# Optimization experiments

Hardware: AMD Instinct MI355X
Metric: run time of the kernel (lower is better)

Reference implementation:

```python
import jax, jax.numpy as jnp
import numpy as np

D = 256; NH = 8; NL = 4; NP = 4; DFF = 2048; HD = D // NH
SHAPES = [(64, 64), (32, 32), (16, 16), (8, 8)]
B = 2; LEN = sum(h * w for h, w in SHAPES)


def setup_inputs() -> dict:
    key = jax.random.key(0)
    ks = jax.random.split(key, 12)
    def w(k, shape, s=0.02):
        return jax.random.normal(k, shape, jnp.float32) * s
    starts = np.cumsum([0] + [h * w for h, w in SHAPES[:-1]])
    return {
        "src": jax.random.normal(ks[0], (B, LEN, D), jnp.float32),
        "pos": jax.random.normal(ks[1], (B, LEN, D), jnp.float32) * 0.1,
        "spatial_shapes": jnp.array(SHAPES, dtype=jnp.int32),
        "level_start_index": jnp.array(starts, dtype=jnp.int32),
        "w_value": w(ks[2], (D, D)), "b_value": jnp.zeros((D,), jnp.float32),
        "w_off": w(ks[3], (D, NH * NL * NP * 2)), "b_off": w(ks[4], (NH * NL * NP * 2,), 0.1),
        "w_attn": w(ks[5], (D, NH * NL * NP)), "b_attn": jnp.zeros((NH * NL * NP,), jnp.float32),
        "w_out": w(ks[6], (D, D)), "b_out": jnp.zeros((D,), jnp.float32),
        "w1": w(ks[7], (D, DFF)), "b1": jnp.zeros((DFF,), jnp.float32),
        "w2": w(ks[8], (DFF, D)), "b2": jnp.zeros((D,), jnp.float32),
        "g1": jnp.ones((D,), jnp.float32), "be1": jnp.zeros((D,), jnp.float32),
        "g2": jnp.ones((D,), jnp.float32), "be2": jnp.zeros((D,), jnp.float32),
    }


def _layer_norm(x, g, b):
    mu = jnp.mean(x, -1, keepdims=True)
    v = jnp.var(x, -1, keepdims=True)
    return (x - mu) * jax.lax.rsqrt(v + 1e-5) * g + b


def _reference_points(shapes):
    # torch.linspace(0.5, H-0.5, H)/H == (arange(H)+0.5)/H
    refs = []
    for H, W in shapes:
        ry = (jnp.arange(H, dtype=jnp.float32) + 0.5) / H
        rx = (jnp.arange(W, dtype=jnp.float32) + 0.5) / W
        yy, xx = jnp.meshgrid(ry, rx, indexing='ij')
        refs.append(jnp.stack([xx.ravel(), yy.ravel()], -1))
    return jnp.concatenate(refs, 0)  # (Len, 2) as (x, y)


def _ms_deform_sample(value, loc, shapes):
    # value: (B, Len, NH, HD); loc: (B, Lq, NH, NL, NP, 2) normalized [0,1]
    # Replicates torch grid_sample(bilinear, padding='zeros', align_corners=False).
    Bn, Lq = loc.shape[0], loc.shape[1]
    P = loc.shape[4]
    start = 0
    outs = []
    for lvl, (H, W) in enumerate(shapes):
        v = value[:, start:start + H * W].transpose(0, 2, 1, 3)  # (B, NH, HW, HD)
        start += H * W
        l = loc[:, :, :, lvl]                      # (B, Lq, NH, P, 2)
        x = l[..., 0] * W - 0.5
        y = l[..., 1] * H - 0.5
        x0 = jnp.floor(x); y0 = jnp.floor(y)
        dx = x - x0; dy = y - y0
        x0i = x0.astype(jnp.int32); y0i = y0.astype(jnp.int32)
        acc = None
        for xi, yi, wgt in ((x0i, y0i, (1 - dx) * (1 - dy)),
                            (x0i + 1, y0i, dx * (1 - dy)),
                            (x0i, y0i + 1, (1 - dx) * dy),
                            (x0i + 1, y0i + 1, dx * dy)):
            valid = ((xi >= 0) & (xi < W) & (yi >= 0) & (yi < H)).astype(value.dtype)
            idx = jnp.clip(yi, 0, H - 1) * W + jnp.clip(xi, 0, W - 1)  # (B, Lq, NH, P)
            idx = idx.transpose(0, 2, 1, 3).reshape(Bn, NH, Lq * P)
            g = jnp.take_along_axis(v, idx[..., None], axis=2).reshape(Bn, NH, Lq, P, HD)
            w = (wgt * valid).transpose(0, 2, 1, 3)[..., None]  # (B, NH, Lq, P, 1)
            acc = g * w if acc is None else acc + g * w
        outs.append(acc)  # (B, NH, Lq, P, HD)
    return jnp.stack(outs, 3)  # (B, NH, Lq, NL, NP, HD)


def _forward(src, pos, w_value, b_value, w_off, b_off, w_attn, b_attn,
             w_out, b_out, w1, b1, w2, b2, g1, be1, g2, be2, shapes):
    Bn, Lq, _ = src.shape
    q = src + pos  # with_pos_embed
    value = (src @ w_value + b_value).reshape(Bn, Lq, NH, HD)
    off = (q @ w_off + b_off).reshape(Bn, Lq, NH, NL, NP, 2)
    attn = jax.nn.softmax((q @ w_attn + b_attn).reshape(Bn, Lq, NH, NL * NP), -1)
    attn = attn.reshape(Bn, Lq, NH, NL, NP)
    ref = _reference_points(shapes)  # (Len, 2)
    normalizer = jnp.array([[w_, h_] for h_, w_ in shapes], jnp.float32)  # (NL, 2) = (W, H)
    loc = ref[None, :, None, None, None, :] + off / normalizer[None, None, None, :, None, :]
    sampled = _ms_deform_sample(value, loc, shapes)  # (B, NH, Lq, NL, NP, HD)
    out = jnp.einsum('bqhlp,bhqlpd->bqhd', attn, sampled).reshape(Bn, Lq, D)
    out = out @ w_out + b_out
    x = _layer_norm(src + out, g1, be1)           # residual + norm1
    ff = jax.nn.relu(x @ w1 + b1) @ w2 + b2       # FFN (dropout=0)
    return _layer_norm(x + ff, g2, be2)           # residual + norm2


def reference(src, pos, spatial_shapes, level_start_index, w_value, b_value,
              w_off, b_off, w_attn, b_attn, w_out, b_out, w1, b1, w2, b2,
              g1, be1, g2, be2):
    shapes = [tuple(int(v) for v in s) for s in np.asarray(spatial_shapes)]
    return _forward(src, pos, w_value, b_value, w_off, b_off, w_attn, b_attn,
                    w_out, b_out, w1, b1, w2, b2, g1, be1, g2, be2, shapes)
```

## Files before the change

### kernel.cpp

```cpp
#include <hip/hip_runtime.h>
#include <math.h>

#define D 256
#define NH 8
#define NL 4
#define NP 4
#define DFF 2048
#define HD 32
#define BB 2
#define LEN 5440
#define MROWS (BB * LEN)

typedef __attribute__((ext_vector_type(8))) short short8;
typedef __attribute__((ext_vector_type(4))) float f32x4;
typedef unsigned int uint32;

__device__ __forceinline__ unsigned short f2bf(float f) {
    uint32 u = __float_as_uint(f);
    u += 0x7FFF + ((u >> 16) & 1);
    return (unsigned short)(u >> 16);
}
__device__ __forceinline__ float bf2f(unsigned short h) {
    return __uint_as_float(((uint32)h) << 16);
}
__device__ __forceinline__ uint32 pack2(float a, float b) {
    return (uint32)f2bf(a) | ((uint32)f2bf(b) << 16);
}

__device__ __forceinline__ void swz85(int b, int ncols, int& row, int& col) {
    const int gsz = ncols << 3;
    const int full = 10 * gsz;
    if (b < full) {
        const int g = b / gsz, idx = b - g * gsz;
        row = (g << 3) + (idx & 7);
        col = idx >> 3;
    } else {
        const int idx = b - full;
        row = 80 + idx % 5;
        col = idx / 5;
    }
}

__global__ void prep(const float* __restrict__ w_value, const float* __restrict__ w_off,
                     const float* __restrict__ w_attn, const float* __restrict__ w_out,
                     const float* __restrict__ w1, const float* __restrict__ w2,
                     const float* __restrict__ b_value, const float* __restrict__ b_off,
                     const float* __restrict__ b_attn,
                     unsigned short* __restrict__ wqvT, unsigned short* __restrict__ woT,
                     unsigned short* __restrict__ w1T, unsigned short* __restrict__ w2T,
                     float* __restrict__ bqv) {
    const int blk = blockIdx.x;
    if (blk >= 1248) {
        for (int i = threadIdx.x; i < 640; i += 256)
            bqv[i] = (i < 256) ? b_value[i] : (i < 512 ? b_off[i - 256] : b_attn[i - 512]);
        return;
    }
    const float* W; unsigned short* WT; int K, N, tid;
    if (blk < 64)       { W = w_value; WT = wqvT;             K = 256;  N = 256;  tid = blk; }
    else if (blk < 128) { W = w_off;   WT = wqvT + 256 * 256; K = 256;  N = 256;  tid = blk - 64; }
    else if (blk < 160) { W = w_attn;  WT = wqvT + 512 * 256; K = 256;  N = 128;  tid = blk - 128; }
    else if (blk < 224) { W = w_out;   WT = woT;              K = 256;  N = 256;  tid = blk - 160; }
    else if (blk < 736) { W = w1;      WT = w1T;              K = 256;  N = 2048; tid = blk - 224; }
    else                { W = w2;      WT = w2T;              K = 2048; N = 256;  tid = blk - 736; }
    const int ntx = N >> 5;
    const int nb = (tid % ntx) * 32, kb = (tid / ntx) * 32;

    __shared__ float tile[32][33];
    const int tx = threadIdx.x & 31, ty = threadIdx.x >> 5;
#pragma unroll
    for (int i = 0; i < 32; i += 8)
        tile[ty + i][tx] = W[(size_t)(kb + ty + i) * N + nb + tx];
    __syncthreads();
#pragma unroll
    for (int i = 0; i < 32; i += 8)
        WT[(size_t)(nb + ty + i) * K + kb + tx] = f2bf(tile[tx][ty + i]);
}

__global__ __launch_bounds__(256) void ffn1_gemm(
        const unsigned short* __restrict__ A,
        const unsigned short* __restrict__ BT, const float* __restrict__ bias,
        unsigned short* __restrict__ Cv, int N, int K, int lda, int ldb) {
    __shared__ unsigned short Ash[128][40];
    __shared__ unsigned short Bsh[128][40];

    int rowt, colt;
    swz85(blockIdx.x, N >> 7, rowt, colt);
    const int row0 = rowt * 128, col0 = colt * 128;

    const int t = threadIdx.x;
    const int wave = t >> 6, lane = t & 63;
    const int wr = wave >> 1, wc = wave & 1;
    const int lrow = lane & 15, quad = lane >> 4;
    const int srow = t >> 1;
    const int cb = (t & 1) * 16;

    const unsigned short* ap = A + (size_t)(row0 + srow) * lda + cb;
    const unsigned short* bp = BT + (size_t)(col0 + srow) * ldb + cb;

    f32x4 acc[4][4];
#pragma unroll
    for (int i = 0; i < 4; i++)
#pragma unroll
        for (int j = 0; j < 4; j++) acc[i][j] = (f32x4){0.f, 0.f, 0.f, 0.f};

    uint4 ra0 = *(const uint4*)(ap + 0), ra1 = *(const uint4*)(ap + 8);
    uint4 rb0 = *(const uint4*)(bp + 0), rb1 = *(const uint4*)(bp + 8);

    for (int kb = 0; kb < K; kb += 32) {
        __syncthreads();
        *(uint4*)&Ash[srow][cb + 0] = ra0;
        *(uint4*)&Ash[srow][cb + 8] = ra1;
        *(uint4*)&Bsh[srow][cb + 0] = rb0;
        *(uint4*)&Bsh[srow][cb + 8] = rb1;
        __syncthreads();
        if (kb + 32 < K) {
            ra0 = *(const uint4*)(ap + kb + 32 + 0);
            ra1 = *(const uint4*)(ap + kb + 32 + 8);
            rb0 = *(const uint4*)(bp + kb + 32 + 0);
            rb1 = *(const uint4*)(bp + kb + 32 + 8);
        }

        short8 af[4], bfr[4];
#pragma unroll
        for (int mt = 0; mt < 4; mt++)
            af[mt] = *(const short8*)&Ash[wr * 64 + mt * 16 + lrow][quad * 8];
#pragma unroll
        for (int nt = 0; nt < 4; nt++)
            bfr[nt] = *(const short8*)&Bsh[wc * 64 + nt * 16 + lrow][quad * 8];
#pragma unroll
        for (int mt = 0; mt < 4; mt++)
#pragma unroll
            for (int nt = 0; nt < 4; nt++)
                acc[mt][nt] = __builtin_amdgcn_mfma_f32_16x16x32_bf16(
                    af[mt], bfr[nt], acc[mt][nt], 0, 0, 0);
    }

#pragma unroll
    for (int nt = 0; nt < 4; nt++) {
        const int col = col0 + wc * 64 + nt * 16 + lrow;
        const float bv = bias[col];
#pragma unroll
        for (int mt = 0; mt < 4; mt++) {
            f32x4 a = acc[mt][nt];
#pragma unroll
            for (int r = 0; r < 4; r++) {
                const int row = row0 + wr * 64 + mt * 16 + quad * 4 + r;
                Cv[(size_t)row * N + col] = f2bf(fmaxf(a[r] + bv, 0.f));
            }
        }
    }
}

template <bool WRITE16>
__global__ __launch_bounds__(256) void gemm_ln(
        const unsigned short* __restrict__ A, const unsigned short* __restrict__ BT,
        const float* __restrict__ bias, const float* __restrict__ rsd,
        const float* __restrict__ g, const float* __restrict__ be,
        float* __restrict__ out, unsigned short* __restrict__ out16, int K) {
    __shared__ __align__(16) unsigned short Ash[32][40];
    __shared__ __align__(16) unsigned short Bsh[256][40];
    __shared__ float red1[4][32], red2[4][32];

    const int row0 = blockIdx.x * 32;
    const int t = threadIdx.x;
    const int wave = t >> 6, lane = t & 63;
    const int lrow = lane & 15, quad = lane >> 4;

    const int ar = t >> 3, ac = (t & 7) * 4;
    const unsigned short* ap = A + (size_t)(row0 + ar) * K + ac;
    const int br = t >> 1, cb = (t & 1) * 16;
    const unsigned short* bp0 = BT + (size_t)br * K + cb;
    const unsigned short* bp1 = BT + (size_t)(128 + br) * K + cb;

    f32x4 acc[2][4];
#pragma unroll
    for (int i = 0; i < 2; i++)
#pragma unroll
        for (int j = 0; j < 4; j++) acc[i][j] = (f32x4){0.f, 0.f, 0.f, 0.f};

    uint2 ra = *(const uint2*)ap;
    uint4 rb00 = *(const uint4*)(bp0 + 0), rb01 = *(const uint4*)(bp0 + 8);
    uint4 rb10 = *(const uint4*)(bp1 + 0), rb11 = *(const uint4*)(bp1 + 8);

    for (int kb = 0; kb < K; kb += 32) {
        __syncthreads();
        *(uint2*)&Ash[ar][ac] = ra;
        *(uint4*)&Bsh[br][cb + 0] = rb00;
        *(uint4*)&Bsh[br][cb + 8] = rb01;
        *(uint4*)&Bsh[128 + br][cb + 0] = rb10;
        *(uint4*)&Bsh[128 + br][cb + 8] = rb11;
        __syncthreads();
        if (kb + 32 < K) {
            ra   = *(const uint2*)(ap + kb + 32);
            rb00 = *(const uint4*)(bp0 + kb + 32 + 0);
            rb01 = *(const uint4*)(bp0 + kb + 32 + 8);
            rb10 = *(const uint4*)(bp1 + kb + 32 + 0);
            rb11 = *(const uint4*)(bp1 + kb + 32 + 8);
        }

        short8 af[2], bfr[4];
#pragma unroll
        for (int mt = 0; mt < 2; mt++)
            af[mt] = *(const short8*)&Ash[mt * 16 + lrow][quad * 8];
#pragma unroll
        for (int nt = 0; nt < 4; nt++)
            bfr[nt] = *(const short8*)&Bsh[wave * 64 + nt * 16 + lrow][quad * 8];
#pragma unroll
        for (int mt = 0; mt < 2; mt++)
#pragma unroll
            for (int nt = 0; nt < 4; nt++)
                acc[mt][nt] = __builtin_amdgcn_mfma_f32_16x16x32_bf16(
                    af[mt], bfr[nt], acc[mt][nt], 0, 0, 0);
    }

    float gv[4], bev[4], bv[4];
#pragma unroll
    for (int nt = 0; nt < 4; nt++) {
        const int col = wave * 64 + nt * 16 + lrow;
        bv[nt] = bias[col];
        gv[nt] = g[col];
        bev[nt] = be[col];
    }

    float v[2][4][4];
#pragma unroll
    for (int mt = 0; mt < 2; mt++)
#pragma unroll
        for (int r = 0; r < 4; r++) {
            const int row = row0 + mt * 16 + quad * 4 + r;
#pragma unroll
            for (int nt = 0; nt < 4; nt++) {
                const int col = wave * 64 + nt * 16 + lrow;
                v[mt][nt][r] = acc[mt][nt][r] + bv[nt] + rsd[(size_t)row * 256 + col];
            }
        }

#pragma unroll
    for (int mt = 0; mt < 2; mt++)
#pragma unroll
        for (int r = 0; r < 4; r++) {
            float s1 = v[mt][0][r] + v[mt][1][r] + v[mt][2][r] + v[mt][3][r];
            float s2 = v[mt][0][r] * v[mt][0][r] + v[mt][1][r] * v[mt][1][r] +
                       v[mt][2][r] * v[mt][2][r] + v[mt][3][r] * v[mt][3][r];
#pragma unroll
            for (int o = 1; o < 16; o <<= 1) {
                s1 += __shfl_xor(s1, o, 16);
                s2 += __shfl_xor(s2, o, 16);
            }
            if (lrow == 0) {
                const int rr = mt * 16 + quad * 4 + r;
                red1[wave][rr] = s1;
                red2[wave][rr] = s2;
            }
        }
    __syncthreads();

#pragma unroll
    for (int mt = 0; mt < 2; mt++)
#pragma unroll
        for (int r = 0; r < 4; r++) {
            const int rr = mt * 16 + quad * 4 + r;
            const float su = red1[0][rr] + red1[1][rr] + red1[2][rr] + red1[3][rr];
            const float sq = red2[0][rr] + red2[1][rr] + red2[2][rr] + red2[3][rr];
            const float mean = su * (1.0f / 256.0f);
            const float var = fmaxf(sq * (1.0f / 256.0f) - mean * mean, 0.f);
            const float rstd = rsqrtf(var + 1e-5f);
            const size_t rowoff = (size_t)(row0 + rr) * 256;
#pragma unroll
            for (int nt = 0; nt < 4; nt++) {
                const int col = wave * 64 + nt * 16 + lrow;
                const float o = (v[mt][nt][r] - mean) * rstd * gv[nt] + bev[nt];
                out[rowoff + col] = o;
                if (WRITE16) out16[rowoff + col] = f2bf(o);
            }
        }
}

__global__ __launch_bounds__(256) void qv_gemm(
        const float* __restrict__ src, const float* __restrict__ pos,
        const unsigned short* __restrict__ BT, const float* __restrict__ bias,
        unsigned short* __restrict__ val, float* __restrict__ qout) {
    __shared__ unsigned short Ash[128][40];
    __shared__ unsigned short Bsh[128][40];

    int rowt, colt;
    swz85(blockIdx.x, 5, rowt, colt);
    const int row0 = rowt * 128, col0 = colt * 128;
    const bool addp = (col0 >= 256);

    const int t = threadIdx.x;
    const int wave = t >> 6, lane = t & 63;
    const int wr = wave >> 1, wc = wave & 1;
    const int lrow = lane & 15, quad = lane >> 4;
    const int srow = t >> 1;
    const int cb = (t & 1) * 16;

    const float* ap = src + (size_t)(row0 + srow) * 256 + cb;
    const float* pp = pos + (size_t)(row0 + srow) * 256 + cb;
    const unsigned short* bp = BT + (size_t)(col0 + srow) * 256 + cb;

    f32x4 acc[4][4];
#pragma unroll
    for (int i = 0; i < 4; i++)
#pragma unroll
        for (int j = 0; j < 4; j++) acc[i][j] = (f32x4){0.f, 0.f, 0.f, 0.f};

    float4 fa[4]; float4 fp[4]; uint4 rb0, rb1;
#pragma unroll
    for (int j = 0; j < 4; j++) fa[j] = *(const float4*)(ap + 4 * j);
    if (addp) {
#pragma unroll
        for (int j = 0; j < 4; j++) fp[j] = *(const float4*)(pp + 4 * j);
    }
    rb0 = *(const uint4*)(bp + 0);
    rb1 = *(const uint4*)(bp + 8);

    for (int kb = 0; kb < 256; kb += 32) {
        __syncthreads();
        {
            float4 f0 = fa[0], f1 = fa[1], f2 = fa[2], f3 = fa[3];
            if (addp) {
                f0.x += fp[0].x; f0.y += fp[0].y; f0.z += fp[0].z; f0.w += fp[0].w;
                f1.x += fp[1].x; f1.y += fp[1].y; f1.z += fp[1].z; f1.w += fp[1].w;
                f2.x += fp[2].x; f2.y += fp[2].y; f2.z += fp[2].z; f2.w += fp[2].w;
                f3.x += fp[3].x; f3.y += fp[3].y; f3.z += fp[3].z; f3.w += fp[3].w;
            }
            uint4 u0 = make_uint4(pack2(f0.x, f0.y), pack2(f0.z, f0.w),
                                  pack2(f1.x, f1.y), pack2(f1.z, f1.w));
            uint4 u1 = make_uint4(pack2(f2.x, f2.y), pack2(f2.z, f2.w),
                                  pack2(f3.x, f3.y), pack2(f3.z, f3.w));
            *(uint4*)&Ash[srow][cb + 0] = u0;
            *(uint4*)&Ash[srow][cb + 8] = u1;
            *(uint4*)&Bsh[srow][cb + 0] = rb0;
            *(uint4*)&Bsh[srow][cb + 8] = rb1;
        }
        __syncthreads();
        if (kb + 32 < 256) {
#pragma unroll
            for (int j = 0; j < 4; j++) fa[j] = *(const float4*)(ap + kb + 32 + 4 * j);
            if (addp) {
#pragma unroll
                for (int j = 0; j < 4; j++) fp[j] = *(const float4*)(pp + kb + 32 + 4 * j);
            }
            rb0 = *(const uint4*)(bp + kb + 32 + 0);
            rb1 = *(const uint4*)(bp + kb + 32 + 8);
        }

        short8 af[4], bfr[4];
#pragma unroll
        for (int mt = 0; mt < 4; mt++)
            af[mt] = *(const short8*)&Ash[wr * 64 + mt * 16 + lrow][quad * 8];
#pragma unroll
        for (int nt = 0; nt < 4; nt++)
            bfr[nt] = *(const short8*)&Bsh[wc * 64 + nt * 16 + lrow][quad * 8];
#pragma unroll
        for (int mt = 0; mt < 4; mt++)
#pragma unroll
            for (int nt = 0; nt < 4; nt++)
                acc[mt][nt] = __builtin_amdgcn_mfma_f32_16x16x32_bf16(
                    af[mt], bfr[nt], acc[mt][nt], 0, 0, 0);
    }

#pragma unroll
    for (int nt = 0; nt < 4; nt++) {
        const int col = col0 + wc * 64 + nt * 16 + lrow;
        const float bv = bias[col];
#pragma unroll
        for (int mt = 0; mt < 4; mt++) {
            f32x4 a = acc[mt][nt];
#pragma unroll
            for (int r = 0; r < 4; r++) {
                const int row = row0 + wr * 64 + mt * 16 + quad * 4 + r;
                float v = a[r] + bv;
                if (col < 256)
                    val[(size_t)row * 256 + col] = f2bf(v);
                else
                    qout[(size_t)row * 384 + (col - 256)] = v;
            }
        }
    }
}

__global__ void sampler(const unsigned short* __restrict__ val, const float* __restrict__ qout,
                        unsigned short* __restrict__ out) {
    __shared__ __align__(16) int   sIdx[2][128][4];
    __shared__ __align__(16) float sW[2][128][4];
    const int t = threadIdx.x;
    const int sub = t >> 7;
    const int tt = t & 127;
    const int bq = blockIdx.x * 2 + sub;
    const int b = bq / LEN, q = bq % LEN;

    {
        const int h = tt >> 4, p = tt & 15;
        const int l = p >> 2;

        float refx, refy;
        if (q < 4096) {
            int rq = q >> 6, cq = q & 63;
            refx = (cq + 0.5f) * (1.0f / 64.0f);
            refy = (rq + 0.5f) * (1.0f / 64.0f);
        } else if (q < 5120) {
            int qq = q - 4096;
            int rq = qq >> 5, cq = qq & 31;
            refx = (cq + 0.5f) * (1.0f / 32.0f);
            refy = (rq + 0.5f) * (1.0f / 32.0f);
        } else if (q < 5376) {
            int qq = q - 5120;
            int rq = qq >> 4, cq = qq & 15;
            refx = (cq + 0.5f) * (1.0f / 16.0f);
            refy = (rq + 0.5f) * (1.0f / 16.0f);
        } else {
            int qq = q - 5376;
            int rq = qq >> 3, cq = qq & 7;
            refx = (cq + 0.5f) * (1.0f / 8.0f);
            refy = (rq + 0.5f) * (1.0f / 8.0f);
        }

        float lv = qout[(size_t)bq * 384 + 256 + tt];
        float mx = lv;
#pragma unroll
        for (int o = 1; o < 16; o <<= 1) mx = fmaxf(mx, __shfl_xor(mx, o, 16));
        float e = expf(lv - mx);
        float s = e;
#pragma unroll
        for (int o = 1; o < 16; o <<= 1) s += __shfl_xor(s, o, 16);
        const float aw = e / s;

        const float ox = qout[(size_t)bq * 384 + h * 32 + p * 2 + 0];
        const float oy = qout[(size_t)bq * 384 + h * 32 + p * 2 + 1];

        const int LST[4] = {0, 4096, 5120, 5376};
        const int WW = 64 >> l;
        const float rw = 1.0f / (float)WW;

        float x = (refx + ox * rw) * (float)WW - 0.5f;
        float y = (refy + oy * rw) * (float)WW - 0.5f;
        float x0f = floorf(x), y0f = floorf(y);
        float dx = x - x0f, dy = y - y0f;
        int x0 = (int)x0f, y0 = (int)y0f;

        const int base = (b * LEN + LST[l]) * 256 + h * 32;
        int xs[2] = {x0, x0 + 1}, ys[2] = {y0, y0 + 1};
        float wx[2] = {1.f - dx, dx}, wy[2] = {1.f - dy, dy};
        int ic[4]; float wc4[4];
#pragma unroll
        for (int cy = 0; cy < 2; cy++)
#pragma unroll
            for (int cx = 0; cx < 2; cx++) {
                int xi = xs[cx], yi = ys[cy];
                bool vld = (xi >= 0) && (xi < WW) && (yi >= 0) && (yi < WW);
                int xc = min(max(xi, 0), WW - 1);
                int yc = min(max(yi, 0), WW - 1);
                ic[cy * 2 + cx] = base + (yc * WW + xc) * 256;
                wc4[cy * 2 + cx] = vld ? wx[cx] * wy[cy] * aw : 0.f;
            }
        *(int4*)&sIdx[sub][tt][0] = make_int4(ic[0], ic[1], ic[2], ic[3]);
        *(float4*)&sW[sub][tt][0] = make_float4(wc4[0], wc4[1], wc4[2], wc4[3]);
    }
    __syncthreads();

    const int h = tt >> 4, dp = tt & 15;
    const unsigned short* vald = val + 2 * dp;
    float acc0 = 0.f, acc1 = 0.f;
#pragma unroll 4
    for (int p = 0; p < 16; p++) {
        const int r = h * 16 + p;
        int4 iv = *(const int4*)&sIdx[sub][r][0];
        float4 wv = *(const float4*)&sW[sub][r][0];
        uint32 u0 = *(const uint32*)(vald + iv.x);
        uint32 u1 = *(const uint32*)(vald + iv.y);
        uint32 u2 = *(const uint32*)(vald + iv.z);
        uint32 u3 = *(const uint32*)(vald + iv.w);
        acc0 += bf2f((unsigned short)u0) * wv.x + bf2f((unsigned short)u1) * wv.y +
                bf2f((unsigned short)u2) * wv.z + bf2f((unsigned short)u3) * wv.w;
        acc1 += bf2f((unsigned short)(u0 >> 16)) * wv.x + bf2f((unsigned short)(u1 >> 16)) * wv.y +
                bf2f((unsigned short)(u2 >> 16)) * wv.z + bf2f((unsigned short)(u3 >> 16)) * wv.w;
    }
    *(uint32*)&out[(size_t)bq * D + h * HD + 2 * dp] = pack2(acc0, acc1);
}

extern "C" void kernel_launch(void* const* d_in, const int* in_sizes, int n_in,
                              void* d_out, int out_size, void* d_ws, size_t ws_size,
                              hipStream_t stream) {
    const float* src     = (const float*)d_in[0];
    const float* pos     = (const float*)d_in[1];
    const float* w_value = (const float*)d_in[4];
    const float* b_value = (const float*)d_in[5];
    const float* w_off   = (const float*)d_in[6];
    const float* b_off   = (const float*)d_in[7];
    const float* w_attn  = (const float*)d_in[8];
    const float* b_attn  = (const float*)d_in[9];
    const float* w_out   = (const float*)d_in[10];
    const float* b_out   = (const float*)d_in[11];
    const float* w1      = (const float*)d_in[12];
    const float* b1      = (const float*)d_in[13];
    const float* w2      = (const float*)d_in[14];
    const float* b2      = (const float*)d_in[15];
    const float* g1      = (const float*)d_in[16];
    const float* be1     = (const float*)d_in[17];
    const float* g2      = (const float*)d_in[18];
    const float* be2     = (const float*)d_in[19];
    float* out = (float*)d_out;

    size_t off = 0;
    auto alloc = [&](size_t bytes) -> char* {
        char* p = (char*)d_ws + off;
        off += (bytes + 255) & ~(size_t)255;
        return p;
    };
    unsigned short* wqvT = (unsigned short*)alloc((size_t)640 * 256 * 2);
    unsigned short* woT  = (unsigned short*)alloc(256 * 256 * 2);
    unsigned short* w1T  = (unsigned short*)alloc((size_t)2048 * 256 * 2);
    unsigned short* w2T  = (unsigned short*)alloc((size_t)256 * 2048 * 2);
    float* bqv           = (float*)alloc(640 * 4);

    float* qout          = (float*)alloc((size_t)MROWS * 384 * 4);
    unsigned short* val  = (unsigned short*)alloc((size_t)MROWS * 256 * 2);
    unsigned short* attn = (unsigned short*)alloc((size_t)MROWS * 256 * 2);
    unsigned short* hb   = (unsigned short*)alloc((size_t)MROWS * 2048 * 2);
    float* xbuf          = (float*)alloc((size_t)MROWS * 256 * 4);
    unsigned short* xb16 = (unsigned short*)alloc((size_t)MROWS * 256 * 2);

    prep<<<1249, 256, 0, stream>>>(w_value, w_off, w_attn, w_out, w1, w2,
                                   b_value, b_off, b_attn, wqvT, woT, w1T, w2T, bqv);

    qv_gemm<<<425, 256, 0, stream>>>(src, pos, wqvT, bqv, val, qout);
    sampler<<<MROWS / 2, 256, 0, stream>>>(val, qout, attn);
    gemm_ln<true><<<340, 256, 0, stream>>>(attn, woT, b_out, src, g1, be1,
                                           xbuf, xb16, 256);

    ffn1_gemm<<<1360, 256, 0, stream>>>(xb16, w1T, b1, hb, 2048, 256, 256, 256);
    gemm_ln<false><<<340, 256, 0, stream>>>(hb, w2T, b2, xbuf, g2, be2,
                                            out, nullptr, 2048);
}
```

Measured before the change: 224.5 us.

## Split FFN2 GEMM over K into four partitions with separate add+LayerNorm reduce

Replaces the fused FFN2 GEMM+LayerNorm kernel, which used 32-row tiles over K=2048 and only 340 blocks, with a split-K GEMM. The new GEMM uses 128x128 tiles and four K-chunks of 512, writing fp32 partials. A separate per-row kernel then sums the partials, adds the bias and residual, and applies LayerNorm. The aim is more parallelism and better tile reuse, at the cost of writing and rereading about 45 MB of fp32 partials plus one extra kernel launch.

```diff
diff --git a/kernel.cpp b/kernel.cpp
--- a/kernel.cpp
+++ b/kernel.cpp
@@ -146,6 +146,84 @@
             for (int r = 0; r < 4; r++) {
                 const int row = row0 + wr * 64 + mt * 16 + quad * 4 + r;
                 Cv[(size_t)row * N + col] = f2bf(fmaxf(a[r] + bv, 0.f));
+            }
+        }
+    }
+}
+
+template <int NZ>
+__global__ __launch_bounds__(256) void splitk_gemm(
+        const unsigned short* __restrict__ A, const unsigned short* __restrict__ BT,
+        float* __restrict__ part, int KC, int lda, int ldb) {
+    __shared__ unsigned short Ash[128][40];
+    __shared__ unsigned short Bsh[128][40];
+
+    int rowt, cc;
+    swz85(blockIdx.x, 2 * NZ, rowt, cc);
+    const int row0 = rowt * 128;
+    const int col0 = (cc & 1) * 128;
+    const int z = cc >> 1;
+    const int koff = z * KC;
+    float* __restrict__ C = part + (size_t)z * MROWS * 256;
+
+    const int t = threadIdx.x;
+    const int wave = t >> 6, lane = t & 63;
+    const int wr = wave >> 1, wc = wave & 1;
+    const int lrow = lane & 15, quad = lane >> 4;
+    const int srow = t >> 1;
+    const int cb = (t & 1) * 16;
+
+    const unsigned short* ap = A + (size_t)(row0 + srow) * lda + koff + cb;
+    const unsigned short* bp = BT + (size_t)(col0 + srow) * ldb + koff + cb;
+
+    f32x4 acc[4][4];
+#pragma unroll
+    for (int i = 0; i < 4; i++)
+#pragma unroll
+        for (int j = 0; j < 4; j++) acc[i][j] = (f32x4){0.f, 0.f, 0.f, 0.f};
+
+    uint4 ra0 = *(const uint4*)(ap + 0), ra1 = *(const uint4*)(ap + 8);
+    uint4 rb0 = *(const uint4*)(bp + 0), rb1 = *(const uint4*)(bp + 8);
+
+    for (int kb = 0; kb < KC; kb += 32) {
+        __syncthreads();
+        *(uint4*)&Ash[srow][cb + 0] = ra0;
+        *(uint4*)&Ash[srow][cb + 8] = ra1;
+        *(uint4*)&Bsh[srow][cb + 0] = rb0;
+        *(uint4*)&Bsh[srow][cb + 8] = rb1;
+        __syncthreads();
+        if (kb + 32 < KC) {
+            ra0 = *(const uint4*)(ap + kb + 32 + 0);
+            ra1 = *(const uint4*)(ap + kb + 32 + 8);
+            rb0 = *(const uint4*)(bp + kb + 32 + 0);
+            rb1 = *(const uint4*)(bp + kb + 32 + 8);
+        }
+
+        short8 af[4], bfr[4];
+#pragma unroll
+        for (int mt = 0; mt < 4; mt++)
+            af[mt] = *(const short8*)&Ash[wr * 64 + mt * 16 + lrow][quad * 8];
+#pragma unroll
+        for (int nt = 0; nt < 4; nt++)
+            bfr[nt] = *(const short8*)&Bsh[wc * 64 + nt * 16 + lrow][quad * 8];
+#pragma unroll
+        for (int mt = 0; mt < 4; mt++)
+#pragma unroll
+            for (int nt = 0; nt < 4; nt++)
+                acc[mt][nt] = __builtin_amdgcn_mfma_f32_16x16x32_bf16(
+                    af[mt], bfr[nt], acc[mt][nt], 0, 0, 0);
+    }
+
+#pragma unroll
+    for (int nt = 0; nt < 4; nt++) {
+        const int col = col0 + wc * 64 + nt * 16 + lrow;
+#pragma unroll
+        for (int mt = 0; mt < 4; mt++) {
+            f32x4 a = acc[mt][nt];
+#pragma unroll
+            for (int r = 0; r < 4; r++) {
+                const int row = row0 + wr * 64 + mt * 16 + quad * 4 + r;
+                C[(size_t)row * 256 + col] = a[r];
             }
         }
     }
@@ -478,6 +556,34 @@
                 bf2f((unsigned short)(u2 >> 16)) * wv.z + bf2f((unsigned short)(u3 >> 16)) * wv.w;
     }
     *(uint32*)&out[(size_t)bq * D + h * HD + 2 * dp] = pack2(acc0, acc1);
+}
+
+template <int NPART>
+__global__ void add_lnN(const float* __restrict__ part, const float* __restrict__ bias,
+                        const float* __restrict__ rsd,
+                        const float* __restrict__ g, const float* __restrict__ be,
+                        float* __restrict__ out, unsigned short* __restrict__ out16) {
+    __shared__ float r1[4], r2[4];
+    const int row = blockIdx.x, t = threadIdx.x;
+    const size_t i = (size_t)row * D + t;
+    float v = bias[t] + rsd[i];
+#pragma unroll
+    for (int z = 0; z < NPART; z++) v += part[(size_t)z * MROWS * 256 + i];
+    float s1 = v, s2 = v * v;
+#pragma unroll
+    for (int o = 32; o > 0; o >>= 1) {
+        s1 += __shfl_down(s1, o, 64);
+        s2 += __shfl_down(s2, o, 64);
+    }
+    if ((t & 63) == 0) { r1[t >> 6] = s1; r2[t >> 6] = s2; }
+    __syncthreads();
+    float su = r1[0] + r1[1] + r1[2] + r1[3];
+    float sq = r2[0] + r2[1] + r2[2] + r2[3];
+    float mean = su * (1.0f / D);
+    float var = fmaxf(sq * (1.0f / D) - mean * mean, 0.f);
+    const float o = (v - mean) * rsqrtf(var + 1e-5f) * g[t] + be[t];
+    out[i] = o;
+    if (out16) out16[i] = f2bf(o);
 }
 
 extern "C" void kernel_launch(void* const* d_in, const int* in_sizes, int n_in,
@@ -521,6 +627,7 @@
     unsigned short* hb   = (unsigned short*)alloc((size_t)MROWS * 2048 * 2);
     float* xbuf          = (float*)alloc((size_t)MROWS * 256 * 4);
     unsigned short* xb16 = (unsigned short*)alloc((size_t)MROWS * 256 * 2);
+    float* part          = (float*)alloc((size_t)4 * MROWS * 256 * 4);
 
     prep<<<1249, 256, 0, stream>>>(w_value, w_off, w_attn, w_out, w1, w2,
                                    b_value, b_off, b_attn, wqvT, woT, w1T, w2T, bqv);
@@ -531,6 +638,6 @@
                                            xbuf, xb16, 256);
 
     ffn1_gemm<<<1360, 256, 0, stream>>>(xb16, w1T, b1, hb, 2048, 256, 256, 256);
-    gemm_ln<false><<<340, 256, 0, stream>>>(hb, w2T, b2, xbuf, g2, be2,
-                                            out, nullptr, 2048);
-}
+    splitk_gemm<4><<<680, 256, 0, stream>>>(hb, w2T, part, 512, 2048, 2048);
+    add_lnN<4><<<MROWS, 256, 0, stream>>>(part, b2, xbuf, g2, be2, out, nullptr);
+}
```

Result: faster. 212.6 us (-5.3%).
